# Performance work log

Measured on AMD Instinct MI355X. Metric: run time of the kernel, lower is better.

## Reference

```python
import jax, jax.numpy as jnp
import numpy as np

ALPHA = 0.2      # LeakyReLU negative slope
NEG = -9e15     # mask fill value, as in pyGAT

B, N, NFEAT, NHID, NCLASS, NHEADS = 4, 2048, 128, 64, 32, 8


def setup_inputs() -> dict:
    key = jax.random.key(0)
    ks = jax.random.split(key, 8)
    x = jax.random.normal(ks[0], (B, N, NFEAT), dtype=jnp.float32)
    adj = jax.random.randint(ks[1], (B, N, N), 0, 2, dtype=jnp.int32)
    W = jax.random.normal(ks[2], (NHEADS, NFEAT, NHID), dtype=jnp.float32) * 0.1
    a1 = jax.random.normal(ks[3], (NHEADS, NHID), dtype=jnp.float32) * 0.1
    a2 = jax.random.normal(ks[4], (NHEADS, NHID), dtype=jnp.float32) * 0.1
    Wo = jax.random.normal(ks[5], (NHEADS * NHID, NCLASS), dtype=jnp.float32) * 0.1
    ao1 = jax.random.normal(ks[6], (NCLASS,), dtype=jnp.float32) * 0.1
    ao2 = jax.random.normal(ks[7], (NCLASS,), dtype=jnp.float32) * 0.1
    return {"x": x, "adj": adj, "W": W, "a1": a1, "a2": a2,
            "Wo": Wo, "ao1": ao1, "ao2": ao2}


def _gat_forward(x, adj, W, a1, a2, Wo, ao1, ao2):
    mask = adj > 0  # [B, N, N]
    # --- multi-head layer (concat=True) ---
    Wh = jnp.einsum('bnf,hfd->bhnd', x, W)          # [B,H,N,nhid]
    f1 = jnp.einsum('bhnd,hd->bhn', Wh, a1)          # Wh @ a[:nhid]
    f2 = jnp.einsum('bhnd,hd->bhn', Wh, a2)          # Wh @ a[nhid:]
    e = jax.nn.leaky_relu(f1[..., :, None] + f2[..., None, :], ALPHA)
    att = jax.nn.softmax(jnp.where(mask[:, None], e, NEG), axis=-1)
    h = jax.nn.elu(jnp.einsum('bhnm,bhmd->bhnd', att, Wh))  # [B,H,N,nhid]
    # torch.cat along dim=2: [B, N, H*nhid]
    h = jnp.transpose(h, (0, 2, 1, 3)).reshape(B, N, NHEADS * NHID)
    # (dropout layers are no-ops in eval mode)
    # --- output head (concat=False, no ELU) ---
    Wh2 = jnp.einsum('bnf,fc->bnc', h, Wo)           # [B,N,nclass]
    g1 = jnp.einsum('bnc,c->bn', Wh2, ao1)
    g2 = jnp.einsum('bnc,c->bn', Wh2, ao2)
    e2 = jax.nn.leaky_relu(g1[:, :, None] + g2[:, None, :], ALPHA)
    att2 = jax.nn.softmax(jnp.where(mask, e2, NEG), axis=-1)
    return jnp.einsum('bnm,bmc->bnc', att2, Wh2)     # [B,N,nclass]


def reference(x, adj, W, a1, a2, Wo, ao1, ao2):
    return _gat_forward(x, adj, W, a1, a2, Wo, ao1, ao2)
```

## Files before the change

### kernel.cpp

```cpp
#include <hip/hip_runtime.h>


typedef _Float16 half8  __attribute__((ext_vector_type(8)));
typedef _Float16 half2_ __attribute__((ext_vector_type(2)));
typedef float  float4_ __attribute__((ext_vector_type(4)));
typedef float  floatx16 __attribute__((ext_vector_type(16)));
typedef unsigned int uint4_ __attribute__((ext_vector_type(4)));

#if __has_builtin(__builtin_amdgcn_exp2f)
#define EXP2(x) __builtin_amdgcn_exp2f(x)
#else
#define EXP2(x) __expf((x) * 0.69314718055994531f)
#endif
#define LOG2E 1.44269504088896340f

static __device__ __forceinline__ unsigned pkh(float a, float b) {
#if __has_builtin(__builtin_amdgcn_cvt_pkrtz)
  return __builtin_bit_cast(unsigned, __builtin_amdgcn_cvt_pkrtz(a, b));
#else
  half2_ h = {(_Float16)a, (_Float16)b};
  return __builtin_bit_cast(unsigned, h);
#endif
}
static __device__ __forceinline__ unsigned short f2h(float f) {
  _Float16 h = (_Float16)f;
  return __builtin_bit_cast(unsigned short, h);
}

static __device__ __forceinline__ unsigned bitm(unsigned mb, int jj) {
#if __has_builtin(__builtin_amdgcn_sbfe)
  return (unsigned)__builtin_amdgcn_sbfe((int)mb, jj, 1);
#else
  return 0u - ((mb >> jj) & 1u);
#endif
}
static __device__ __forceinline__ unsigned pmask(unsigned s0, unsigned s1) {
  return __builtin_amdgcn_perm(s1, s0, 0x05040100u);
}
static __device__ __forceinline__ unsigned wmaxh(unsigned u, unsigned u2,
    unsigned pm, half2_ Ah, half2_ A2h) {
  half2_ p = Ah * __builtin_bit_cast(half2_, u);
  half2_ n = A2h * __builtin_bit_cast(half2_, u2);
  half2_ m = __builtin_elementwise_max(p, n);
  return __builtin_bit_cast(unsigned, m) & pm;
}

__global__ __launch_bounds__(256) void k_wfrag(
    const float* __restrict__ Wm, const float* __restrict__ Wo,
    unsigned short* __restrict__ Wf, unsigned short* __restrict__ WoF) {
  if (blockIdx.x < 32) {
    const int T = blockIdx.x * 256 + threadIdx.x;
    const int lane = T & 63;
    int r = T >> 6;
    const int nt = r & 3; r >>= 2;
    const int kstep = r & 3; r >>= 2;
    const int h = r;
    const int kk = kstep * 32 + (lane >> 4) * 8;
    const int n = nt * 16 + (lane & 15);
    const float* sp = Wm + h * 8192 + kk * 64 + n;
    unsigned short o[8];
    #pragma unroll
    for (int jj = 0; jj < 8; ++jj) o[jj] = f2h(sp[jj * 64]);
    *(uint4_*)(Wf + T * 8) = *(uint4_*)o;
  } else {
    const int T = (blockIdx.x - 32) * 256 + threadIdx.x;
    const int lane = T & 63;
    const int nt = (T >> 6) & 1, kstep = T >> 7;
    const int kk = kstep * 32 + (lane >> 4) * 8;
    const int n = nt * 16 + (lane & 15);
    unsigned short o[8];
    #pragma unroll
    for (int jj = 0; jj < 8; ++jj) o[jj] = f2h(Wo[(kk + jj) * 32 + n]);
    *(uint4_*)(WoF + T * 8) = *(uint4_*)o;
  }
}

__global__ __launch_bounds__(256) void k_front(
    const int* __restrict__ adj, unsigned long long* __restrict__ maskb,
    const float* __restrict__ x, const unsigned short* __restrict__ Wf,
    const float* __restrict__ a1, const float* __restrict__ a2,
    unsigned short* __restrict__ WhF, float* __restrict__ f1,
    unsigned short* __restrict__ Uv, unsigned short* __restrict__ U2v) {
  __shared__ float wsm[64 * 68];
  const int bx = blockIdx.x;
  const int t = threadIdx.x;
  if (bx >= 1024) {
    const int lane = t & 63, wid = t >> 6;
    const int s = lane & 15;
    const long long row0 = (long long)(bx - 1024) * 4;
    for (int rr = 0; rr < 4; ++rr) {
      const long long row = row0 + rr;
      const int4* src = (const int4*)(adj + row * 2048);
      #pragma unroll
      for (int c = 0; c < 2; ++c) {
        int4 v = src[c * 256 + t];
        unsigned nib = (v.x != 0 ? 1u : 0u) | (v.y != 0 ? 2u : 0u) |
                       (v.z != 0 ? 4u : 0u) | (v.w != 0 ? 8u : 0u);
        unsigned lo = (s < 8) ? (nib << (s * 4)) : 0u;
        unsigned hi = (s >= 8) ? (nib << ((s - 8) * 4)) : 0u;
        #pragma unroll
        for (int off = 1; off < 16; off <<= 1) {
          lo |= __shfl_xor(lo, off);
          hi |= __shfl_xor(hi, off);
        }
        if (s == 0) {
          const int word = c * 16 + wid * 4 + (lane >> 4);
          maskb[(((row >> 11) * 32 + word) << 11) + (row & 2047)] =
              ((unsigned long long)hi << 32) | (unsigned long long)lo;
        }
      }
    }
    return;
  }
  const int itile = bx & 31, bh = bx >> 5;
  const int b = bh >> 3, h = bh & 7;
  const int i0 = itile * 64;
  const int lane = t & 63, w = t >> 6;
  const int cl = lane & 15, q = lane >> 4;
  const float* xrow = x + ((long long)b * 2048 + i0 + w * 16 + cl) * 128;
  const unsigned short* wfh = Wf + h * 8192;
  float4_ acc0 = {0.f, 0.f, 0.f, 0.f}, acc1 = acc0, acc2 = acc0, acc3 = acc0;
  #pragma unroll
  for (int kstep = 0; kstep < 4; ++kstep) {
    const float* xp = xrow + kstep * 32 + q * 8;
    const float4 xa = *(const float4*)xp;
    const float4 xb = *(const float4*)(xp + 4);
    uint4_ ap;
    ap.x = pkh(xa.x, xa.y);
    ap.y = pkh(xa.z, xa.w);
    ap.z = pkh(xb.x, xb.y);
    ap.w = pkh(xb.z, xb.w);
    const half8 af = __builtin_bit_cast(half8, ap);
    const unsigned short* bp = wfh + kstep * 2048 + lane * 8;
    const half8 b0 = *(const half8*)(bp);
    const half8 b1 = *(const half8*)(bp + 512);
    const half8 b2 = *(const half8*)(bp + 1024);
    const half8 b3 = *(const half8*)(bp + 1536);
    acc0 = __builtin_amdgcn_mfma_f32_16x16x32_f16(af, b0, acc0, 0, 0, 0);
    acc1 = __builtin_amdgcn_mfma_f32_16x16x32_f16(af, b1, acc1, 0, 0, 0);
    acc2 = __builtin_amdgcn_mfma_f32_16x16x32_f16(af, b2, acc2, 0, 0, 0);
    acc3 = __builtin_amdgcn_mfma_f32_16x16x32_f16(af, b3, acc3, 0, 0, 0);
  }
  {
    float4_ accs[4] = {acc0, acc1, acc2, acc3};
    #pragma unroll
    for (int nt = 0; nt < 4; ++nt)
      #pragma unroll
      for (int reg = 0; reg < 4; ++reg)
        wsm[(w * 16 + q * 4 + reg) * 68 + nt * 16 + cl] = accs[nt][reg];
  }
  __syncthreads();
  {
    const int row = t >> 2, seg = t & 3;
    const float* wr = wsm + row * 68 + seg * 16;
    const float4* a1p = (const float4*)(a1 + h * 64 + seg * 16);
    const float4* a2p = (const float4*)(a2 + h * 64 + seg * 16);
    float p1 = 0.f, p2 = 0.f;
    #pragma unroll
    for (int u = 0; u < 4; ++u) {
      const float4 wv = *(const float4*)(wr + u * 4);
      const float4 v1 = a1p[u];
      const float4 v2 = a2p[u];
      p1 += wv.x * v1.x + wv.y * v1.y + wv.z * v1.z + wv.w * v1.w;
      p2 += wv.x * v2.x + wv.y * v2.y + wv.z * v2.z + wv.w * v2.w;
    }
    p1 += __shfl_xor(p1, 1); p1 += __shfl_xor(p1, 2);
    p2 += __shfl_xor(p2, 1); p2 += __shfl_xor(p2, 2);
    if (seg == 0) {
      f1[(long long)bh * 2048 + i0 + row] = p1 * LOG2E;
      const float s2 = p2 * LOG2E;
      Uv[(long long)bh * 2048 + i0 + row] = f2h(EXP2(s2));
      U2v[(long long)bh * 2048 + i0 + row] = f2h(EXP2(0.2f * s2));
    }
  }
  #pragma unroll
  for (int u = 0; u < 2; ++u) {
    const int idx = u * 256 + t;
    const int l2 = idx & 63, df = (idx >> 6) & 1, jbs = idx >> 7;
    const int jrow = jbs * 16 + (l2 >> 5) * 8;
    const int d = df * 32 + (l2 & 31);
    uint4_ o;
    o.x = pkh(wsm[(jrow + 0) * 68 + d], wsm[(jrow + 1) * 68 + d]);
    o.y = pkh(wsm[(jrow + 2) * 68 + d], wsm[(jrow + 3) * 68 + d]);
    o.z = pkh(wsm[(jrow + 4) * 68 + d], wsm[(jrow + 5) * 68 + d]);
    o.w = pkh(wsm[(jrow + 6) * 68 + d], wsm[(jrow + 7) * 68 + d]);
    const long long off = (long long)bh * 131072 +
                          ((long long)itile * 4 + jbs) * 1024 + df * 512 + l2 * 8;
    *(uint4_*)(WhF + off) = o;
  }
}

__global__ __launch_bounds__(256, 4) void k_attn1(
    const unsigned short* __restrict__ whf, const float* __restrict__ f1v,
    const unsigned short* __restrict__ Uv, const unsigned short* __restrict__ U2v,
    const unsigned long long* __restrict__ maskb, unsigned short* __restrict__ hA) {
  __shared__ __align__(16) unsigned short bsm[2][8448];
  const int bh = blockIdx.y, b = bh >> 3, hh = bh & 7;
  const int t = threadIdx.x;
  const int lane = t & 63, w = t >> 6;
  const int cl = lane & 31;
  const int qh = lane >> 5, qs2 = qh * 8;
  const long long rbase = (long long)bh * 2048;
  const int row_l = blockIdx.x * 128 + w * 32 + cl;
  const float f1i = f1v[rbase + row_l];
  const float A = EXP2(f1i), A2 = EXP2(0.2f * f1i);
  const half2_ Ah = __builtin_bit_cast(half2_, pkh(A, A));
  const half2_ A2h = __builtin_bit_cast(half2_, pkh(A2, A2));
  const uint2* mT = (const uint2*)maskb;
  const long long mbase = (long long)b * 65536 + row_l;
  const unsigned short* whfb = whf + (long long)bh * 131072;
  const float4* gB = (const float4*)whfb;
  const unsigned* usrc = (const unsigned*)((t < 64 ? Uv : U2v) + rbase) + (t & 63);
  const half8 vones = {1.0f16, 1.0f16, 1.0f16, 1.0f16, 1.0f16, 1.0f16, 1.0f16, 1.0f16};
  const floatx16 zero16 = {0.f, 0.f, 0.f, 0.f, 0.f, 0.f, 0.f, 0.f,
                           0.f, 0.f, 0.f, 0.f, 0.f, 0.f, 0.f, 0.f};
  floatx16 acc0 = zero16, acc1 = zero16, az = zero16;
  {
    const float4* gp = gB + t;
    float4 s0 = gp[0], s1 = gp[256], s2 = gp[512], s3 = gp[768];
    float4* dp = (float4*)bsm[0] + t;
    dp[0] = s0; dp[256] = s1; dp[512] = s2; dp[768] = s3;
    if (t < 128) ((unsigned*)bsm[0])[4096 + t] = usrc[0];
  }
  uint2 mw0_c = mT[mbase], mw1_c = mT[mbase + 2048];
  for (int s = 0; s < 16; ++s) {
    __syncthreads();
    const int sn = (s < 15) ? (s + 1) : 15;
    float4 st0, st1, st2, st3;
    {
      const float4* gp = gB + sn * 1024 + t;
      st0 = gp[0]; st1 = gp[256]; st2 = gp[512]; st3 = gp[768];
    }
    unsigned ustg = 0;
    if (t < 128) ustg = usrc[sn * 64];
    const uint2 mwA = mw0_c, mwB = mw1_c;
    mw0_c = mT[mbase + (long long)(sn * 2) * 2048];
    mw1_c = mT[mbase + (long long)(sn * 2 + 1) * 2048];
    const unsigned short* bs = bsm[s & 1];
    #pragma unroll
    for (int ks = 0; ks < 8; ++ks) {
      const uint2 mwu = (ks < 4) ? mwA : mwB;
      const unsigned mword = (ks & 2) ? mwu.y : mwu.x;
      const unsigned mb = mword >> (((ks & 1) << 4) + qs2);
      const uint4_ uv  = *(const uint4_*)(bs + 8192 + ks * 16 + qs2);
      const uint4_ u2v = *(const uint4_*)(bs + 8320 + ks * 16 + qs2);
      const unsigned short* bp = bs + ks * 1024 + lane * 8;
      const half8 b0 = *(const half8*)(bp);
      const half8 b1 = *(const half8*)(bp + 512);
      const unsigned s0 = bitm(mb, 0), s1 = bitm(mb, 1), s2 = bitm(mb, 2),
                     s3 = bitm(mb, 3), s4 = bitm(mb, 4), s5 = bitm(mb, 5),
                     s6 = bitm(mb, 6), s7 = bitm(mb, 7);
      uint4_ pk;
      pk.x = wmaxh(uv.x, u2v.x, pmask(s0, s1), Ah, A2h);
      pk.y = wmaxh(uv.y, u2v.y, pmask(s2, s3), Ah, A2h);
      pk.z = wmaxh(uv.z, u2v.z, pmask(s4, s5), Ah, A2h);
      pk.w = wmaxh(uv.w, u2v.w, pmask(s6, s7), Ah, A2h);
      const half8 af = __builtin_bit_cast(half8, pk);
      __builtin_amdgcn_s_setprio(1);
      acc0 = __builtin_amdgcn_mfma_f32_32x32x16_f16(af, b0, acc0, 0, 0, 0);
      acc1 = __builtin_amdgcn_mfma_f32_32x32x16_f16(af, b1, acc1, 0, 0, 0);
      az   = __builtin_amdgcn_mfma_f32_32x32x16_f16(af, vones, az, 0, 0, 0);
      __builtin_amdgcn_s_setprio(0);
    }
    if (s < 15) {
      float4* dp = (float4*)bsm[(s + 1) & 1] + t;
      dp[0] = st0; dp[256] = st1; dp[512] = st2; dp[768] = st3;
      if (t < 128) ((unsigned*)bsm[(s + 1) & 1])[4096 + t] = ustg;
    }
  }
  __syncthreads();
  float* hs = (float*)bsm;
  #pragma unroll
  for (int reg = 0; reg < 16; ++reg) {
    const int crow = (reg & 3) + 8 * (reg >> 2) + 4 * qh;
    const float rz = 1.f / az[reg];
    float v0 = acc0[reg] * rz;
    v0 = (v0 > 0.f) ? v0 : (__expf(v0) - 1.f);
    hs[(w * 32 + crow) * 66 + cl] = v0;
    float v1 = acc1[reg] * rz;
    v1 = (v1 > 0.f) ? v1 : (__expf(v1) - 1.f);
    hs[(w * 32 + crow) * 66 + 32 + cl] = v1;
  }
  __syncthreads();
  const int rtg0 = b * 128 + blockIdx.x * 8;
  #pragma unroll
  for (int u = 0; u < 4; ++u) {
    const int id = u * 256 + t;
    const int l2 = id & 63, ks2 = (id >> 6) & 1, rtile = id >> 7;
    const int rowl = rtile * 16 + (l2 & 15);
    const int d = ks2 * 32 + (l2 >> 4) * 8;
    const float* hp = hs + rowl * 66 + d;
    uint4_ o;
    o.x = pkh(hp[0], hp[1]); o.y = pkh(hp[2], hp[3]);
    o.z = pkh(hp[4], hp[5]); o.w = pkh(hp[6], hp[7]);
    const long long rt = rtg0 + rtile;
    const int kstep = hh * 2 + ks2;
    *(uint4_*)(hA + ((rt * 16 + kstep) * 64 + l2) * 8) = o;
  }
}

__global__ __launch_bounds__(128) void k_ogemm(
    const unsigned short* __restrict__ hA, const unsigned short* __restrict__ WoF,
    const float* __restrict__ ao1, const float* __restrict__ ao2,
    unsigned short* __restrict__ Wh2F, float* __restrict__ g1,
    unsigned short* __restrict__ gU, unsigned short* __restrict__ gU2) {
  __shared__ float w2s[32 * 36];
  const int t = threadIdx.x, lane = t & 63, wv = t >> 6;
  const int cl = lane & 15, q = lane >> 4;
  const long long rt = (long long)blockIdx.x * 2 + wv;
  float4_ acc0 = {0.f, 0.f, 0.f, 0.f}, acc1 = acc0;
  const unsigned short* ap = hA + rt * 8192 + lane * 8;
  const unsigned short* bp = WoF + lane * 8;
  #pragma unroll
  for (int kstep = 0; kstep < 16; ++kstep) {
    const half8 af = *(const half8*)(ap + kstep * 512);
    const half8 b0 = *(const half8*)(bp + kstep * 1024);
    const half8 b1 = *(const half8*)(bp + kstep * 1024 + 512);
    acc0 = __builtin_amdgcn_mfma_f32_16x16x32_f16(af, b0, acc0, 0, 0, 0);
    acc1 = __builtin_amdgcn_mfma_f32_16x16x32_f16(af, b1, acc1, 0, 0, 0);
  }
  const float o1a = ao1[cl], o1b = ao1[cl + 16];
  const float o2a = ao2[cl], o2b = ao2[cl + 16];
  #pragma unroll
  for (int reg = 0; reg < 4; ++reg) {
    const int rowl = wv * 16 + q * 4 + reg;
    w2s[rowl * 36 + cl] = acc0[reg];
    w2s[rowl * 36 + 16 + cl] = acc1[reg];
    float p1 = acc0[reg] * o1a + acc1[reg] * o1b;
    float p2 = acc0[reg] * o2a + acc1[reg] * o2b;
    p1 += __shfl_xor(p1, 1); p1 += __shfl_xor(p1, 2);
    p1 += __shfl_xor(p1, 4); p1 += __shfl_xor(p1, 8);
    p2 += __shfl_xor(p2, 1); p2 += __shfl_xor(p2, 2);
    p2 += __shfl_xor(p2, 4); p2 += __shfl_xor(p2, 8);
    if (cl == 0) {
      const long long row = (long long)blockIdx.x * 32 + rowl;
      g1[row] = p1 * LOG2E;
      const float s2 = p2 * LOG2E;
      gU[row]  = f2h(EXP2(s2));
      gU2[row] = f2h(EXP2(0.2f * s2));
    }
  }
  __syncthreads();
  {
    const int l2 = t & 63, nt2 = t >> 6;
    const int g = blockIdx.x >> 6, jc = (blockIdx.x >> 1) & 31, ks2 = blockIdx.x & 1;
    const int kb = (l2 >> 4) * 8, n = nt2 * 16 + (l2 & 15);
    uint4_ o;
    o.x = pkh(w2s[(kb + 0) * 36 + n], w2s[(kb + 1) * 36 + n]);
    o.y = pkh(w2s[(kb + 2) * 36 + n], w2s[(kb + 3) * 36 + n]);
    o.z = pkh(w2s[(kb + 4) * 36 + n], w2s[(kb + 5) * 36 + n]);
    o.w = pkh(w2s[(kb + 6) * 36 + n], w2s[(kb + 7) * 36 + n]);
    const long long off = (long long)g * 65536 + jc * 2048 + ks2 * 1024 +
                          nt2 * 512 + l2 * 8;
    *(uint4_*)(Wh2F + off) = o;
  }
}

__global__ __launch_bounds__(256) void k_attn2(
    const unsigned short* __restrict__ whf2, const float* __restrict__ g1v,
    const unsigned short* __restrict__ gU, const unsigned short* __restrict__ gU2,
    const unsigned long long* __restrict__ maskb, float* __restrict__ outp) {
  __shared__ float accs[4][16][33];
  __shared__ float zsh[64];
  const int b = blockIdx.y;
  const long long i0 = (long long)blockIdx.x * 16;
  const int t = threadIdx.x, lane = t & 63, wid = t >> 6;
  const int cl = lane & 15, q = lane >> 4;
  const float g1i = g1v[(long long)b * 2048 + i0 + cl];
  const float A = EXP2(g1i), A2 = EXP2(0.2f * g1i);
  const half2_ Ah = __builtin_bit_cast(half2_, pkh(A, A));
  const half2_ A2h = __builtin_bit_cast(half2_, pkh(A2, A2));
  const uint2* mT = (const uint2*)maskb;
  const int mrow = (int)(i0 + cl);
  const long long mbase = (long long)b * 65536 + mrow;
  const unsigned short* ub = gU + (long long)b * 2048;
  const unsigned short* u2b = gU2 + (long long)b * 2048;
  const unsigned short* wb = whf2 + (long long)b * 65536;
  const half8 vones = {1.0f16, 1.0f16, 1.0f16, 1.0f16, 1.0f16, 1.0f16, 1.0f16, 1.0f16};
  float4_ acc0 = {0.f, 0.f, 0.f, 0.f}, acc1 = acc0, accz = acc0;
  const int qs = q * 8;
  const int jc0 = wid * 8;
  uint2 mw_c = mT[mbase + (long long)jc0 * 2048];
  uint4_ ua_c  = *(const uint4_*)(ub  + jc0 * 64 + qs);
  uint4_ u2a_c = *(const uint4_*)(u2b + jc0 * 64 + qs);
  uint4_ ubn_c  = *(const uint4_*)(ub  + jc0 * 64 + 32 + qs);
  uint4_ u2b_c = *(const uint4_*)(u2b + jc0 * 64 + 32 + qs);
  for (int c8 = 0; c8 < 8; ++c8) {
    const int jc = jc0 + c8;
    const uint2 mw = mw_c;
    const uint4_ uA = ua_c, u2A = u2a_c, uB = ubn_c, u2B = u2b_c;
    {
      const int jn = jc + ((c8 < 7) ? 1 : 0);
      mw_c = mT[mbase + (long long)jn * 2048];
      ua_c  = *(const uint4_*)(ub  + jn * 64 + qs);
      u2a_c = *(const uint4_*)(u2b + jn * 64 + qs);
      ubn_c  = *(const uint4_*)(ub  + jn * 64 + 32 + qs);
      u2b_c = *(const uint4_*)(u2b + jn * 64 + 32 + qs);
    }
    const unsigned short* bb = wb + (jc * 2) * 1024 + lane * 8;
    #pragma unroll
    for (int ks = 0; ks < 2; ++ks) {
      const unsigned mb = (ks ? mw.y : mw.x) >> qs;
      const uint4_ uv  = ks ? uB : uA;
      const uint4_ u2v = ks ? u2B : u2A;
      const unsigned s0 = bitm(mb, 0), s1 = bitm(mb, 1), s2 = bitm(mb, 2),
                     s3 = bitm(mb, 3), s4 = bitm(mb, 4), s5 = bitm(mb, 5),
                     s6 = bitm(mb, 6), s7 = bitm(mb, 7);
      uint4_ pk;
      pk.x = wmaxh(uv.x, u2v.x, pmask(s0, s1), Ah, A2h);
      pk.y = wmaxh(uv.y, u2v.y, pmask(s2, s3), Ah, A2h);
      pk.z = wmaxh(uv.z, u2v.z, pmask(s4, s5), Ah, A2h);
      pk.w = wmaxh(uv.w, u2v.w, pmask(s6, s7), Ah, A2h);
      const half8 af = __builtin_bit_cast(half8, pk);
      const unsigned short* bk = bb + ks * 1024;
      const half8 b0 = *(const half8*)bk;
      const half8 b1 = *(const half8*)(bk + 512);
      acc0 = __builtin_amdgcn_mfma_f32_16x16x32_f16(af, b0, acc0, 0, 0, 0);
      acc1 = __builtin_amdgcn_mfma_f32_16x16x32_f16(af, b1, acc1, 0, 0, 0);
      accz = __builtin_amdgcn_mfma_f32_16x16x32_f16(af, vones, accz, 0, 0, 0);
    }
  }
  if (cl == 0) {
    #pragma unroll
    for (int reg = 0; reg < 4; ++reg) zsh[wid * 16 + q * 4 + reg] = accz[reg];
  }
  float4_ a01[2] = {acc0, acc1};
  #pragma unroll
  for (int nt = 0; nt < 2; ++nt)
    #pragma unroll
    for (int reg = 0; reg < 4; ++reg)
      accs[wid][q * 4 + reg][nt * 16 + cl] = a01[nt][reg];
  __syncthreads();
  #pragma unroll
  for (int r = 0; r < 2; ++r) {
    int o = r * 256 + t;
    int il = o >> 5, c = o & 31;
    float s = accs[0][il][c] + accs[1][il][c] + accs[2][il][c] + accs[3][il][c];
    float Z = zsh[il] + zsh[16 + il] + zsh[32 + il] + zsh[48 + il];
    outp[((long long)b * 2048 + i0 + il) * 32 + c] = s / Z;
  }
}

extern "C" void kernel_launch(void* const* d_in, const int* in_sizes, int n_in,
                              void* d_out, int out_size, void* d_ws, size_t ws_size,
                              hipStream_t stream) {
  const float* x   = (const float*)d_in[0];
  const int*   adj = (const int*)d_in[1];
  const float* W   = (const float*)d_in[2];
  const float* a1  = (const float*)d_in[3];
  const float* a2  = (const float*)d_in[4];
  const float* Wo  = (const float*)d_in[5];
  const float* ao1 = (const float*)d_in[6];
  const float* ao2 = (const float*)d_in[7];
  float* out = (float*)d_out;
  char* ws = (char*)d_ws;

  unsigned long long* maskb = (unsigned long long*)(ws + 0);
  unsigned short* Wf   = (unsigned short*)(ws + 2097152);
  unsigned short* WoF  = (unsigned short*)(ws + 2228224);
  unsigned short* WhF  = (unsigned short*)(ws + 18874368);
  float* f1   = (float*)(ws + 27262976);
  unsigned short* Uv  = (unsigned short*)(ws + 27525120);
  unsigned short* U2v = (unsigned short*)(ws + 27656192);
  unsigned short* hA  = (unsigned short*)(ws + 27787264);
  unsigned short* Wh2F = (unsigned short*)(ws + 45613056);
  float* g1   = (float*)(ws + 46137344);
  unsigned short* gU  = (unsigned short*)(ws + 46170112);
  unsigned short* gU2 = (unsigned short*)(ws + 46186496);

  hipLaunchKernelGGL(k_wfrag, dim3(40), dim3(256), 0, stream, W, Wo, Wf, WoF);
  hipLaunchKernelGGL(k_front, dim3(3072), dim3(256), 0, stream, adj, maskb,
                     x, Wf, a1, a2, WhF, f1, Uv, U2v);
  hipLaunchKernelGGL(k_attn1, dim3(16, 32), dim3(256), 0, stream, WhF, f1, Uv, U2v,
                     maskb, hA);
  hipLaunchKernelGGL(k_ogemm, dim3(256), dim3(128), 0, stream, hA, WoF, ao1, ao2,
                     Wh2F, g1, gU, gU2);
  hipLaunchKernelGGL(k_attn2, dim3(128, 4), dim3(256), 0, stream, Wh2F, g1, gU, gU2,
                     maskb, out);
}
```

Baseline: 165.9 us.

## Split attention key range across wave pairs and replace rowsum MFMA with fdot2

k_attn1 now gives each block 64 query rows instead of 128. Two waves cover the two halves of each 32-key-step range for the same rows, and their partial accumulators are reduced through shared memory. The grid doubles to 1024 blocks, which is meant to improve occupancy and load balance. The third MFMA that computed the softmax denominator is replaced with fdot2 partial sums plus a cross-lane shuffle, cutting matrix-core work by a third. In exchange the kernel gains an extra shared-memory reduction pass and another sync, and each block reloads the full Wh tile for half as many rows.

```diff
diff --git a/kernel.cpp b/kernel.cpp
--- a/kernel.cpp
+++ b/kernel.cpp
@@ -43,6 +43,15 @@
   half2_ n = A2h * __builtin_bit_cast(half2_, u2);
   half2_ m = __builtin_elementwise_max(p, n);
   return __builtin_bit_cast(unsigned, m) & pm;
+}
+static __device__ __forceinline__ float dot2z(unsigned pw, float acc) {
+  const half2_ h = __builtin_bit_cast(half2_, pw);
+#if __has_builtin(__builtin_amdgcn_fdot2)
+  const half2_ ones2 = {1.0f16, 1.0f16};
+  return __builtin_amdgcn_fdot2(h, ones2, acc, false);
+#else
+  return acc + (float)h[0] + (float)h[1];
+#endif
 }
 
 __global__ __launch_bounds__(256) void k_wfrag(
@@ -194,14 +203,15 @@
     const unsigned short* __restrict__ whf, const float* __restrict__ f1v,
     const unsigned short* __restrict__ Uv, const unsigned short* __restrict__ U2v,
     const unsigned long long* __restrict__ maskb, unsigned short* __restrict__ hA) {
-  __shared__ __align__(16) unsigned short bsm[2][8448];
+  __shared__ __align__(16) unsigned short bsm[2][2][4224];
   const int bh = blockIdx.y, b = bh >> 3, hh = bh & 7;
   const int t = threadIdx.x;
   const int lane = t & 63, w = t >> 6;
+  const int jh = w & 1, rg = w >> 1;
   const int cl = lane & 31;
   const int qh = lane >> 5, qs2 = qh * 8;
   const long long rbase = (long long)bh * 2048;
-  const int row_l = blockIdx.x * 128 + w * 32 + cl;
+  const int row_l = blockIdx.x * 64 + rg * 32 + cl;
   const float f1i = f1v[rbase + row_l];
   const float A = EXP2(f1i), A2 = EXP2(0.2f * f1i);
   const half2_ Ah = __builtin_bit_cast(half2_, pkh(A, A));
@@ -209,41 +219,43 @@
   const uint2* mT = (const uint2*)maskb;
   const long long mbase = (long long)b * 65536 + row_l;
   const unsigned short* whfb = whf + (long long)bh * 131072;
-  const float4* gB = (const float4*)whfb;
-  const unsigned* usrc = (const unsigned*)((t < 64 ? Uv : U2v) + rbase) + (t & 63);
-  const half8 vones = {1.0f16, 1.0f16, 1.0f16, 1.0f16, 1.0f16, 1.0f16, 1.0f16, 1.0f16};
+  const int jh_t = t >> 7, tl = t & 127;
+  const float4* gBh = (const float4*)whfb + jh_t * 8192;
+  const int ju = (t >> 6) & 1, us = (t >> 5) & 1, ui = t & 31;
+  const unsigned* usrc =
+      (const unsigned*)((us ? U2v : Uv) + rbase) + ju * 512 + ui;
   const floatx16 zero16 = {0.f, 0.f, 0.f, 0.f, 0.f, 0.f, 0.f, 0.f,
                            0.f, 0.f, 0.f, 0.f, 0.f, 0.f, 0.f, 0.f};
-  floatx16 acc0 = zero16, acc1 = zero16, az = zero16;
+  floatx16 acc0 = zero16, acc1 = zero16;
+  float z0 = 0.f, z1 = 0.f, z2 = 0.f, z3 = 0.f;
   {
-    const float4* gp = gB + t;
-    float4 s0 = gp[0], s1 = gp[256], s2 = gp[512], s3 = gp[768];
-    float4* dp = (float4*)bsm[0] + t;
-    dp[0] = s0; dp[256] = s1; dp[512] = s2; dp[768] = s3;
-    if (t < 128) ((unsigned*)bsm[0])[4096 + t] = usrc[0];
-  }
-  uint2 mw0_c = mT[mbase], mw1_c = mT[mbase + 2048];
+    const float4* gp = gBh + tl;
+    const float4 s0 = gp[0], s1 = gp[128], s2 = gp[256], s3 = gp[384];
+    float4* dp = (float4*)((char*)bsm + jh_t * 8448) + tl;
+    dp[0] = s0; dp[128] = s1; dp[256] = s2; dp[384] = s3;
+    if (t < 128)
+      *(unsigned*)((char*)bsm + ju * 8448 + 8192 + us * 128 + ui * 4) = usrc[0];
+  }
+  uint2 mw_c = mT[mbase + (long long)(jh * 16) * 2048];
   for (int s = 0; s < 16; ++s) {
     __syncthreads();
     const int sn = (s < 15) ? (s + 1) : 15;
     float4 st0, st1, st2, st3;
     {
-      const float4* gp = gB + sn * 1024 + t;
-      st0 = gp[0]; st1 = gp[256]; st2 = gp[512]; st3 = gp[768];
+      const float4* gp = gBh + sn * 512 + tl;
+      st0 = gp[0]; st1 = gp[128]; st2 = gp[256]; st3 = gp[384];
     }
     unsigned ustg = 0;
-    if (t < 128) ustg = usrc[sn * 64];
-    const uint2 mwA = mw0_c, mwB = mw1_c;
-    mw0_c = mT[mbase + (long long)(sn * 2) * 2048];
-    mw1_c = mT[mbase + (long long)(sn * 2 + 1) * 2048];
-    const unsigned short* bs = bsm[s & 1];
-    #pragma unroll
-    for (int ks = 0; ks < 8; ++ks) {
-      const uint2 mwu = (ks < 4) ? mwA : mwB;
-      const unsigned mword = (ks & 2) ? mwu.y : mwu.x;
+    if (t < 128) ustg = usrc[sn * 32];
+    const uint2 mw = mw_c;
+    mw_c = mT[mbase + (long long)(jh * 16 + sn) * 2048];
+    const unsigned short* bs = &bsm[s & 1][jh][0];
+    #pragma unroll
+    for (int ks = 0; ks < 4; ++ks) {
+      const unsigned mword = (ks & 2) ? mw.y : mw.x;
       const unsigned mb = mword >> (((ks & 1) << 4) + qs2);
-      const uint4_ uv  = *(const uint4_*)(bs + 8192 + ks * 16 + qs2);
-      const uint4_ u2v = *(const uint4_*)(bs + 8320 + ks * 16 + qs2);
+      const uint4_ uv  = *(const uint4_*)(bs + 4096 + ks * 16 + qs2);
+      const uint4_ u2v = *(const uint4_*)(bs + 4160 + ks * 16 + qs2);
       const unsigned short* bp = bs + ks * 1024 + lane * 8;
       const half8 b0 = *(const half8*)(bp);
       const half8 b1 = *(const half8*)(bp + 512);
@@ -259,37 +271,49 @@
       __builtin_amdgcn_s_setprio(1);
       acc0 = __builtin_amdgcn_mfma_f32_32x32x16_f16(af, b0, acc0, 0, 0, 0);
       acc1 = __builtin_amdgcn_mfma_f32_32x32x16_f16(af, b1, acc1, 0, 0, 0);
-      az   = __builtin_amdgcn_mfma_f32_32x32x16_f16(af, vones, az, 0, 0, 0);
       __builtin_amdgcn_s_setprio(0);
+      z0 = dot2z(pk.x, z0); z1 = dot2z(pk.y, z1);
+      z2 = dot2z(pk.z, z2); z3 = dot2z(pk.w, z3);
     }
     if (s < 15) {
-      float4* dp = (float4*)bsm[(s + 1) & 1] + t;
-      dp[0] = st0; dp[256] = st1; dp[512] = st2; dp[768] = st3;
-      if (t < 128) ((unsigned*)bsm[(s + 1) & 1])[4096 + t] = ustg;
+      char* nb = (char*)bsm + ((s + 1) & 1) * 16896;
+      float4* dp = (float4*)(nb + jh_t * 8448) + tl;
+      dp[0] = st0; dp[128] = st1; dp[256] = st2; dp[384] = st3;
+      if (t < 128) *(unsigned*)(nb + ju * 8448 + 8192 + us * 128 + ui * 4) = ustg;
     }
   }
   __syncthreads();
   float* hs = (float*)bsm;
+  float zl = z0 + z1 + z2 + z3;
+  zl += __shfl_xor(zl, 32);
   #pragma unroll
   for (int reg = 0; reg < 16; ++reg) {
     const int crow = (reg & 3) + 8 * (reg >> 2) + 4 * qh;
-    const float rz = 1.f / az[reg];
-    float v0 = acc0[reg] * rz;
-    v0 = (v0 > 0.f) ? v0 : (__expf(v0) - 1.f);
-    hs[(w * 32 + crow) * 66 + cl] = v0;
-    float v1 = acc1[reg] * rz;
-    v1 = (v1 > 0.f) ? v1 : (__expf(v1) - 1.f);
-    hs[(w * 32 + crow) * 66 + 32 + cl] = v1;
-  }
+    const int row = rg * 32 + crow;
+    hs[jh * 4160 + row * 65 + cl] = acc0[reg];
+    hs[jh * 4160 + row * 65 + 32 + cl] = acc1[reg];
+  }
+  if (qh == 0) hs[8320 + jh * 64 + rg * 32 + cl] = zl;
   __syncthreads();
-  const int rtg0 = b * 128 + blockIdx.x * 8;
-  #pragma unroll
-  for (int u = 0; u < 4; ++u) {
+  #pragma unroll
+  for (int i = 0; i < 16; ++i) {
+    const int idx = i * 256 + t;
+    const int row = idx >> 6, d = idx & 63;
+    const float v = hs[row * 65 + d] + hs[4160 + row * 65 + d];
+    const float Z = hs[8320 + row] + hs[8384 + row];
+    float hv = v / Z;
+    hv = (hv > 0.f) ? hv : (__expf(hv) - 1.f);
+    hs[row * 65 + d] = hv;
+  }
+  __syncthreads();
+  const int rtg0 = b * 128 + blockIdx.x * 4;
+  #pragma unroll
+  for (int u = 0; u < 2; ++u) {
     const int id = u * 256 + t;
     const int l2 = id & 63, ks2 = (id >> 6) & 1, rtile = id >> 7;
     const int rowl = rtile * 16 + (l2 & 15);
     const int d = ks2 * 32 + (l2 >> 4) * 8;
-    const float* hp = hs + rowl * 66 + d;
+    const float* hp = hs + rowl * 65 + d;
     uint4_ o;
     o.x = pkh(hp[0], hp[1]); o.y = pkh(hp[2], hp[3]);
     o.z = pkh(hp[4], hp[5]); o.w = pkh(hp[6], hp[7]);
@@ -471,7 +495,7 @@
   hipLaunchKernelGGL(k_wfrag, dim3(40), dim3(256), 0, stream, W, Wo, Wf, WoF);
   hipLaunchKernelGGL(k_front, dim3(3072), dim3(256), 0, stream, adj, maskb,
                      x, Wf, a1, a2, WhF, f1, Uv, U2v);
-  hipLaunchKernelGGL(k_attn1, dim3(16, 32), dim3(256), 0, stream, WhF, f1, Uv, U2v,
+  hipLaunchKernelGGL(k_attn1, dim3(32, 32), dim3(256), 0, stream, WhF, f1, Uv, U2v,
                      maskb, hA);
   hipLaunchKernelGGL(k_ogemm, dim3(256), dim3(128), 0, stream, hA, WoF, ao1, ao2,
                      Wh2F, g1, gU, gU2);
```

Result: slower. 169.4 us (+2.1%).

## Split attention K dimension across waves, 64-row blocks, dot2 row-sum

Applied to the files above, without the earlier changes.

Restructures k_attn1 so each block handles 64 rows instead of 128. The four waves now split the key (j) dimension of each stage rather than the rows, and partial accumulators are reduced through shared memory. The softmax denominator comes from fdot2 row sums instead of an extra MFMA against a ones vector, and the grid doubles to 1024 blocks. This cuts MFMA work and raises block count for occupancy, at the cost of an LDS cross-wave reduction, a larger shared buffer and more registers.

```diff
diff --git a/kernel.cpp b/kernel.cpp
--- a/kernel.cpp
+++ b/kernel.cpp
@@ -43,6 +43,15 @@
   half2_ n = A2h * __builtin_bit_cast(half2_, u2);
   half2_ m = __builtin_elementwise_max(p, n);
   return __builtin_bit_cast(unsigned, m) & pm;
+}
+static __device__ __forceinline__ float dot2z(unsigned pw, float acc) {
+  const half2_ h = __builtin_bit_cast(half2_, pw);
+#if __has_builtin(__builtin_amdgcn_fdot2)
+  const half2_ ones2 = {1.0f16, 1.0f16};
+  return __builtin_amdgcn_fdot2(h, ones2, acc, false);
+#else
+  return acc + (float)h[0] + (float)h[1];
+#endif
 }
 
 __global__ __launch_bounds__(256) void k_wfrag(
@@ -194,35 +203,43 @@
     const unsigned short* __restrict__ whf, const float* __restrict__ f1v,
     const unsigned short* __restrict__ Uv, const unsigned short* __restrict__ U2v,
     const unsigned long long* __restrict__ maskb, unsigned short* __restrict__ hA) {
-  __shared__ __align__(16) unsigned short bsm[2][8448];
+  __shared__ __align__(16) unsigned short bsm[2][16896];
   const int bh = blockIdx.y, b = bh >> 3, hh = bh & 7;
   const int t = threadIdx.x;
-  const int lane = t & 63, w = t >> 6;
+  const int lane = t & 63, q = t >> 6;
   const int cl = lane & 31;
   const int qh = lane >> 5, qs2 = qh * 8;
   const long long rbase = (long long)bh * 2048;
-  const int row_l = blockIdx.x * 128 + w * 32 + cl;
-  const float f1i = f1v[rbase + row_l];
-  const float A = EXP2(f1i), A2 = EXP2(0.2f * f1i);
-  const half2_ Ah = __builtin_bit_cast(half2_, pkh(A, A));
-  const half2_ A2h = __builtin_bit_cast(half2_, pkh(A2, A2));
-  const uint2* mT = (const uint2*)maskb;
-  const long long mbase = (long long)b * 65536 + row_l;
+  const int row0 = blockIdx.x * 64 + cl;
+  const float f10 = f1v[rbase + row0];
+  const float f11 = f1v[rbase + row0 + 32];
+  const float A0 = EXP2(f10), A20 = EXP2(0.2f * f10);
+  const float A1 = EXP2(f11), A21 = EXP2(0.2f * f11);
+  const half2_ Ah0  = __builtin_bit_cast(half2_, pkh(A0, A0));
+  const half2_ A2h0 = __builtin_bit_cast(half2_, pkh(A20, A20));
+  const half2_ Ah1  = __builtin_bit_cast(half2_, pkh(A1, A1));
+  const half2_ A2h1 = __builtin_bit_cast(half2_, pkh(A21, A21));
+  const unsigned* mask32 = (const unsigned*)maskb;
+  const long long mq = (((long long)b * 32 + (q >> 1)) * 2048 + row0) * 2 + (q & 1);
   const unsigned short* whfb = whf + (long long)bh * 131072;
   const float4* gB = (const float4*)whfb;
-  const unsigned* usrc = (const unsigned*)((t < 64 ? Uv : U2v) + rbase) + (t & 63);
-  const half8 vones = {1.0f16, 1.0f16, 1.0f16, 1.0f16, 1.0f16, 1.0f16, 1.0f16, 1.0f16};
+  const int ju = t >> 6 >= 2 ? 0 : 0;
+  const int sju = (t >> 6) & 1, sui = t & 63;
+  const unsigned* usrc =
+      (const unsigned*)((sju ? U2v : Uv) + rbase) + sui;
   const floatx16 zero16 = {0.f, 0.f, 0.f, 0.f, 0.f, 0.f, 0.f, 0.f,
                            0.f, 0.f, 0.f, 0.f, 0.f, 0.f, 0.f, 0.f};
-  floatx16 acc0 = zero16, acc1 = zero16, az = zero16;
+  floatx16 acc00 = zero16, acc01 = zero16;
+  floatx16 acc10 = zero16, acc11 = zero16;
+  float zA = 0.f, zB = 0.f;
   {
     const float4* gp = gB + t;
-    float4 s0 = gp[0], s1 = gp[256], s2 = gp[512], s3 = gp[768];
+    const float4 s0 = gp[0], s1 = gp[256], s2 = gp[512], s3 = gp[768];
     float4* dp = (float4*)bsm[0] + t;
     dp[0] = s0; dp[256] = s1; dp[512] = s2; dp[768] = s3;
-    if (t < 128) ((unsigned*)bsm[0])[4096 + t] = usrc[0];
-  }
-  uint2 mw0_c = mT[mbase], mw1_c = mT[mbase + 2048];
+    if (t < 128) ((unsigned*)bsm[0])[4096 + sju * 64 + sui] = usrc[0];
+  }
+  unsigned m0_c = mask32[mq], m1_c = mask32[mq + 64];
   for (int s = 0; s < 16; ++s) {
     __syncthreads();
     const int sn = (s < 15) ? (s + 1) : 15;
@@ -233,63 +250,114 @@
     }
     unsigned ustg = 0;
     if (t < 128) ustg = usrc[sn * 64];
-    const uint2 mwA = mw0_c, mwB = mw1_c;
-    mw0_c = mT[mbase + (long long)(sn * 2) * 2048];
-    mw1_c = mT[mbase + (long long)(sn * 2 + 1) * 2048];
+    const unsigned mw0 = m0_c, mw1 = m1_c;
+    m0_c = mask32[mq + (long long)sn * 8192];
+    m1_c = mask32[mq + (long long)sn * 8192 + 64];
     const unsigned short* bs = bsm[s & 1];
     #pragma unroll
-    for (int ks = 0; ks < 8; ++ks) {
-      const uint2 mwu = (ks < 4) ? mwA : mwB;
-      const unsigned mword = (ks & 2) ? mwu.y : mwu.x;
-      const unsigned mb = mword >> (((ks & 1) << 4) + qs2);
-      const uint4_ uv  = *(const uint4_*)(bs + 8192 + ks * 16 + qs2);
-      const uint4_ u2v = *(const uint4_*)(bs + 8320 + ks * 16 + qs2);
-      const unsigned short* bp = bs + ks * 1024 + lane * 8;
+    for (int ks = 0; ks < 2; ++ks) {
+      const int jo = q * 32 + ks * 16;
+      const uint4_ uv  = *(const uint4_*)(bs + 8192 + jo + qs2);
+      const uint4_ u2v = *(const uint4_*)(bs + 8320 + jo + qs2);
+      const unsigned short* bp = bs + (q * 2 + ks) * 1024 + lane * 8;
       const half8 b0 = *(const half8*)(bp);
       const half8 b1 = *(const half8*)(bp + 512);
-      const unsigned s0 = bitm(mb, 0), s1 = bitm(mb, 1), s2 = bitm(mb, 2),
-                     s3 = bitm(mb, 3), s4 = bitm(mb, 4), s5 = bitm(mb, 5),
-                     s6 = bitm(mb, 6), s7 = bitm(mb, 7);
-      uint4_ pk;
-      pk.x = wmaxh(uv.x, u2v.x, pmask(s0, s1), Ah, A2h);
-      pk.y = wmaxh(uv.y, u2v.y, pmask(s2, s3), Ah, A2h);
-      pk.z = wmaxh(uv.z, u2v.z, pmask(s4, s5), Ah, A2h);
-      pk.w = wmaxh(uv.w, u2v.w, pmask(s6, s7), Ah, A2h);
-      const half8 af = __builtin_bit_cast(half8, pk);
-      __builtin_amdgcn_s_setprio(1);
-      acc0 = __builtin_amdgcn_mfma_f32_32x32x16_f16(af, b0, acc0, 0, 0, 0);
-      acc1 = __builtin_amdgcn_mfma_f32_32x32x16_f16(af, b1, acc1, 0, 0, 0);
-      az   = __builtin_amdgcn_mfma_f32_32x32x16_f16(af, vones, az, 0, 0, 0);
-      __builtin_amdgcn_s_setprio(0);
+      const int sh = ks * 16 + qs2;
+      {
+        const unsigned mb = mw0 >> sh;
+        const unsigned s0 = bitm(mb, 0), s1 = bitm(mb, 1), s2 = bitm(mb, 2),
+                       s3 = bitm(mb, 3), s4 = bitm(mb, 4), s5 = bitm(mb, 5),
+                       s6 = bitm(mb, 6), s7 = bitm(mb, 7);
+        uint4_ pk;
+        pk.x = wmaxh(uv.x, u2v.x, pmask(s0, s1), Ah0, A2h0);
+        pk.y = wmaxh(uv.y, u2v.y, pmask(s2, s3), Ah0, A2h0);
+        pk.z = wmaxh(uv.z, u2v.z, pmask(s4, s5), Ah0, A2h0);
+        pk.w = wmaxh(uv.w, u2v.w, pmask(s6, s7), Ah0, A2h0);
+        const half8 af = __builtin_bit_cast(half8, pk);
+        __builtin_amdgcn_s_setprio(1);
+        acc00 = __builtin_amdgcn_mfma_f32_32x32x16_f16(af, b0, acc00, 0, 0, 0);
+        acc01 = __builtin_amdgcn_mfma_f32_32x32x16_f16(af, b1, acc01, 0, 0, 0);
+        __builtin_amdgcn_s_setprio(0);
+        zA = dot2z(pk.x, zA); zA = dot2z(pk.y, zA);
+        zA = dot2z(pk.z, zA); zA = dot2z(pk.w, zA);
+      }
+      {
+        const unsigned mb = mw1 >> sh;
+        const unsigned s0 = bitm(mb, 0), s1 = bitm(mb, 1), s2 = bitm(mb, 2),
+                       s3 = bitm(mb, 3), s4 = bitm(mb, 4), s5 = bitm(mb, 5),
+                       s6 = bitm(mb, 6), s7 = bitm(mb, 7);
+        uint4_ pk;
+        pk.x = wmaxh(uv.x, u2v.x, pmask(s0, s1), Ah1, A2h1);
+        pk.y = wmaxh(uv.y, u2v.y, pmask(s2, s3), Ah1, A2h1);
+        pk.z = wmaxh(uv.z, u2v.z, pmask(s4, s5), Ah1, A2h1);
+        pk.w = wmaxh(uv.w, u2v.w, pmask(s6, s7), Ah1, A2h1);
+        const half8 af = __builtin_bit_cast(half8, pk);
+        __builtin_amdgcn_s_setprio(1);
+        acc10 = __builtin_amdgcn_mfma_f32_32x32x16_f16(af, b0, acc10, 0, 0, 0);
+        acc11 = __builtin_amdgcn_mfma_f32_32x32x16_f16(af, b1, acc11, 0, 0, 0);
+        __builtin_amdgcn_s_setprio(0);
+        zB = dot2z(pk.x, zB); zB = dot2z(pk.y, zB);
+        zB = dot2z(pk.z, zB); zB = dot2z(pk.w, zB);
+      }
     }
     if (s < 15) {
       float4* dp = (float4*)bsm[(s + 1) & 1] + t;
       dp[0] = st0; dp[256] = st1; dp[512] = st2; dp[768] = st3;
-      if (t < 128) ((unsigned*)bsm[(s + 1) & 1])[4096 + t] = ustg;
+      if (t < 128) ((unsigned*)bsm[(s + 1) & 1])[4096 + sju * 64 + sui] = ustg;
     }
   }
   __syncthreads();
   float* hs = (float*)bsm;
-  #pragma unroll
-  for (int reg = 0; reg < 16; ++reg) {
-    const int crow = (reg & 3) + 8 * (reg >> 2) + 4 * qh;
-    const float rz = 1.f / az[reg];
-    float v0 = acc0[reg] * rz;
-    v0 = (v0 > 0.f) ? v0 : (__expf(v0) - 1.f);
-    hs[(w * 32 + crow) * 66 + cl] = v0;
-    float v1 = acc1[reg] * rz;
-    v1 = (v1 > 0.f) ? v1 : (__expf(v1) - 1.f);
-    hs[(w * 32 + crow) * 66 + 32 + cl] = v1;
-  }
-  __syncthreads();
-  const int rtg0 = b * 128 + blockIdx.x * 8;
-  #pragma unroll
-  for (int u = 0; u < 4; ++u) {
+  zA += __shfl_xor(zA, 32);
+  zB += __shfl_xor(zB, 32);
+  if (qh == 0) {
+    hs[8192 + q * 64 + cl] = zA;
+    hs[8192 + q * 64 + 32 + cl] = zB;
+  }
+  if (q < 2) {
+    float* r = hs + q * 4096;
+    #pragma unroll
+    for (int reg = 0; reg < 16; ++reg) {
+      const int crow = (reg & 3) + 8 * (reg >> 2) + 4 * qh;
+      r[crow * 64 + cl] = acc00[reg];
+      r[crow * 64 + 32 + cl] = acc01[reg];
+      r[(crow + 32) * 64 + cl] = acc10[reg];
+      r[(crow + 32) * 64 + 32 + cl] = acc11[reg];
+    }
+  }
+  __syncthreads();
+  if (q >= 2) {
+    float* r = hs + (q - 2) * 4096;
+    #pragma unroll
+    for (int reg = 0; reg < 16; ++reg) {
+      const int crow = (reg & 3) + 8 * (reg >> 2) + 4 * qh;
+      r[crow * 64 + cl] += acc00[reg];
+      r[crow * 64 + 32 + cl] += acc01[reg];
+      r[(crow + 32) * 64 + cl] += acc10[reg];
+      r[(crow + 32) * 64 + 32 + cl] += acc11[reg];
+    }
+  }
+  __syncthreads();
+  #pragma unroll
+  for (int i = 0; i < 16; ++i) {
+    const int idx = i * 256 + t;
+    const int row = idx >> 6;
+    const float v = hs[idx] + hs[4096 + idx];
+    const float Z = hs[8192 + row] + hs[8256 + row] +
+                    hs[8320 + row] + hs[8384 + row];
+    float hv = v / Z;
+    hv = (hv > 0.f) ? hv : (__expf(hv) - 1.f);
+    hs[idx] = hv;
+  }
+  __syncthreads();
+  const int rtg0 = b * 128 + blockIdx.x * 4;
+  #pragma unroll
+  for (int u = 0; u < 2; ++u) {
     const int id = u * 256 + t;
     const int l2 = id & 63, ks2 = (id >> 6) & 1, rtile = id >> 7;
     const int rowl = rtile * 16 + (l2 & 15);
     const int d = ks2 * 32 + (l2 >> 4) * 8;
-    const float* hp = hs + rowl * 66 + d;
+    const float* hp = hs + rowl * 64 + d;
     uint4_ o;
     o.x = pkh(hp[0], hp[1]); o.y = pkh(hp[2], hp[3]);
     o.z = pkh(hp[4], hp[5]); o.w = pkh(hp[6], hp[7]);
@@ -471,7 +539,7 @@
   hipLaunchKernelGGL(k_wfrag, dim3(40), dim3(256), 0, stream, W, Wo, Wf, WoF);
   hipLaunchKernelGGL(k_front, dim3(3072), dim3(256), 0, stream, adj, maskb,
                      x, Wf, a1, a2, WhF, f1, Uv, U2v);
-  hipLaunchKernelGGL(k_attn1, dim3(16, 32), dim3(256), 0, stream, WhF, f1, Uv, U2v,
+  hipLaunchKernelGGL(k_attn1, dim3(32, 32), dim3(256), 0, stream, WhF, f1, Uv, U2v,
                      maskb, hA);
   hipLaunchKernelGGL(k_ogemm, dim3(256), dim3(128), 0, stream, hA, WoF, ao1, ao2,
                      Wh2F, g1, gU, gU2);
```

Result: slower. 171.5 us (+3.4%).
